# Optimization experiments

Measured on AMD Instinct MI355X. Metric: run time of the kernel, lower is better.

Reference implementation:

```python
import jax, jax.numpy as jnp
import numpy as np

B, C_IN, C_OUT, H, W = 8, 4, 64, 8, 2048


def setup_inputs() -> dict:
    key = jax.random.key(0)
    ks = jax.random.split(key, 7)
    # torch Conv2d default init: U(-s, s) with s = 1/sqrt(fan_in), fan_in = C_in*1*1
    s = 1.0 / np.sqrt(C_IN)
    u = lambda k, shape: jax.random.uniform(k, shape, jnp.float32, -s, s)
    return {
        "x": jax.random.normal(ks[0], (B, C_IN, H, W), jnp.float32),
        "Wq": u(ks[1], (C_OUT, C_IN)), "bq": u(ks[2], (C_OUT,)),
        "Wk": u(ks[3], (C_OUT, C_IN)), "bk": u(ks[4], (C_OUT,)),
        "Wv": u(ks[5], (C_OUT, C_IN)), "bv": u(ks[6], (C_OUT,)),
        "causal": 1,
    }


def reference(x, Wq, bq, Wk, bk, Wv, bv, causal):
    b, c_in, h, w = x.shape
    # 1x1 conv == per-pixel linear over channel axis
    def proj(Wm, bm):
        y = jnp.einsum('bchw,oc->bohw', x, Wm) + bm[None, :, None, None]
        return y.reshape(b, -1, w)              # [B, C_out*H, W]
    Q = proj(Wq, bq)
    K = proj(Wk, bk)
    V = proj(Wv, bv)
    d = Q.shape[1]
    # scores[b,k,l] = sum_d Q[b,d,k] * K[b,d,l] / sqrt(d)   -> [B, W, W]
    scores = jnp.einsum('bdk,bdl->bkl', Q, K) / (float(d) ** 0.5)
    if causal:
        # faithful to torch: triu zeros lower triangle, then any zero -> -inf
        scores = jnp.triu(scores)
        scores = jnp.where(scores != 0, scores, -jnp.inf)
    attn = jax.nn.softmax(scores, axis=-1)
    # x_out[b,d,k] = sum_l V[b,d,l] * attn[b,k,l]
    x_out = jnp.einsum('bdl,bkl->bdk', V, attn).reshape(b, -1, h, w)
    return x_out, scores  # plot_weight is the pre-softmax (masked) scores
```

## Files before the change

kernel.cpp:

```cpp
#include <hip/hip_runtime.h>
#include <math.h>


#define B_ 8
#define W_ 2048
#define D_ 512
#define SCALE_ 0.04419417382415922f
#define NEG_BIG_ (-3.0e38f)

typedef __attribute__((ext_vector_type(8))) short bf16x8;
typedef __attribute__((ext_vector_type(4))) float f32x4;

__device__ __forceinline__ unsigned short f2bf(float x) {
  unsigned int u = __float_as_uint(x);
  u += 0x7fffu + ((u >> 16) & 1u);
  return (unsigned short)(u >> 16);
}
__device__ __forceinline__ float bf2f(unsigned short h) {
  return __uint_as_float(((unsigned int)h) << 16);
}
__device__ __forceinline__ void split2(float x, unsigned short& hi, unsigned short& lo) {
  hi = f2bf(x);
  lo = f2bf(x - bf2f(hi));
}

__device__ __forceinline__ void gl16(const unsigned short* g, unsigned short* l) {
  __builtin_amdgcn_global_load_lds(
      (__attribute__((address_space(1))) void*)const_cast<unsigned short*>(g),
      (__attribute__((address_space(3))) void*)l, 16, 0, 0);
}

__device__ __forceinline__ int swz(int row, int lq) {
  return row * 32 + ((lq ^ ((row >> 1) & 3)) << 3);
}

__global__ __launch_bounds__(256) void proj_qk(
    const float* __restrict__ x,
    const float* __restrict__ Wq, const float* __restrict__ bq,
    const float* __restrict__ Wk, const float* __restrict__ bk,
    unsigned short* __restrict__ Qhi, unsigned short* __restrict__ Qlo,
    unsigned short* __restrict__ Khi, unsigned short* __restrict__ Klo) {
  int idx = blockIdx.x * 256 + threadIdx.x;
  int o = idx & 63;
  int w = (idx >> 6) & (W_ - 1);
  int b = idx >> 17;
  const float* xb = x + (size_t)b * 32 * W_ + w;
  float xv[4][8];
#pragma unroll
  for (int c = 0; c < 4; c++)
#pragma unroll
    for (int h = 0; h < 8; h++) xv[c][h] = xb[(c * 8 + h) * W_];
  float wq0 = Wq[o * 4], wq1 = Wq[o * 4 + 1], wq2 = Wq[o * 4 + 2], wq3 = Wq[o * 4 + 3];
  float wk0 = Wk[o * 4], wk1 = Wk[o * 4 + 1], wk2 = Wk[o * 4 + 2], wk3 = Wk[o * 4 + 3];
  float bqv = bq[o], bkv = bk[o];
  unsigned short qh8[8] __attribute__((aligned(16))), ql8[8] __attribute__((aligned(16)));
  unsigned short kh8[8] __attribute__((aligned(16))), kl8[8] __attribute__((aligned(16)));
#pragma unroll
  for (int h = 0; h < 8; h++) {
    float q = bqv + wq0 * xv[0][h] + wq1 * xv[1][h] + wq2 * xv[2][h] + wq3 * xv[3][h];
    float k = bkv + wk0 * xv[0][h] + wk1 * xv[1][h] + wk2 * xv[2][h] + wk3 * xv[3][h];
    split2(q, qh8[h], ql8[h]);
    split2(k, kh8[h], kl8[h]);
  }
  size_t base = ((size_t)b * W_ + w) * D_ + o * 8;
  *(uint4*)&Qhi[base] = *(uint4*)qh8;
  *(uint4*)&Qlo[base] = *(uint4*)ql8;
  *(uint4*)&Khi[base] = *(uint4*)kh8;
  *(uint4*)&Klo[base] = *(uint4*)kl8;
}

__global__ __launch_bounds__(256) void proj_v(
    const float* __restrict__ x,
    const float* __restrict__ Wv, const float* __restrict__ bv,
    unsigned short* __restrict__ Vhi, unsigned short* __restrict__ Vlo) {
  int idx = blockIdx.x * 256 + threadIdx.x;
  int wc = idx & 255;
  int d = (idx >> 8) & (D_ - 1);
  int b = idx >> 17;
  int o = d >> 3, h = d & 7;
  const float* xp = x + ((size_t)(b * 4) * 8 + h) * W_ + wc * 8;
  float4 xa[4][2];
#pragma unroll
  for (int c = 0; c < 4; c++) {
    xa[c][0] = *(const float4*)&xp[(size_t)c * 8 * W_];
    xa[c][1] = *(const float4*)&xp[(size_t)c * 8 * W_ + 4];
  }
  float w0 = Wv[o * 4], w1 = Wv[o * 4 + 1], w2 = Wv[o * 4 + 2], w3 = Wv[o * 4 + 3];
  float bvv = bv[o];
  unsigned short vh8[8] __attribute__((aligned(16))), vl8[8] __attribute__((aligned(16)));
#pragma unroll
  for (int j = 0; j < 8; j++) {
    float x0 = (j < 4) ? ((const float*)&xa[0][0])[j] : ((const float*)&xa[0][1])[j - 4];
    float x1 = (j < 4) ? ((const float*)&xa[1][0])[j] : ((const float*)&xa[1][1])[j - 4];
    float x2 = (j < 4) ? ((const float*)&xa[2][0])[j] : ((const float*)&xa[2][1])[j - 4];
    float x3 = (j < 4) ? ((const float*)&xa[3][0])[j] : ((const float*)&xa[3][1])[j - 4];
    float v = bvv + w0 * x0 + w1 * x1 + w2 * x2 + w3 * x3;
    split2(v, vh8[j], vl8[j]);
  }
  size_t base = ((size_t)b * D_ + d) * W_ + wc * 8;
  *(uint4*)&Vhi[base] = *(uint4*)vh8;
  *(uint4*)&Vlo[base] = *(uint4*)vl8;
}

__global__ __launch_bounds__(256) void scores_mfma(
    const unsigned short* __restrict__ Qhi, const unsigned short* __restrict__ Qlo,
    const unsigned short* __restrict__ Khi, const unsigned short* __restrict__ Klo,
    float* __restrict__ S, float2* __restrict__ stats, const int* __restrict__ causal_p) {
  int f = (blockIdx.z * 16 + blockIdx.y) * 16 + blockIdx.x;
  int lf = (f & 7) * 256 + (f >> 3);
  int b = lf >> 8;
  int k0 = ((lf >> 4) & 15) * 128;
  int l0 = (lf & 15) * 128;
  int causal = *causal_p;
  int t = threadIdx.x;
  float* Sb = S + (size_t)b * W_ * W_;

  if (causal && (l0 + 127 < k0)) {
    float4 nb = make_float4(NEG_BIG_, NEG_BIG_, NEG_BIG_, NEG_BIG_);
    int row = t >> 1, c0 = (t & 1) * 64;
#pragma unroll
    for (int j = 0; j < 16; j++)
      *(float4*)&Sb[(size_t)(k0 + row) * W_ + l0 + c0 + j * 4] = nb;
    return;
  }

  __shared__ __align__(16) unsigned short qh_s[128 * 32], ql_s[128 * 32];
  __shared__ __align__(16) unsigned short kh_s[128 * 32], kl_s[128 * 32];
  __shared__ float sm_h[2][128], ss_h[2][128];

  int wave = t >> 6, lane = t & 63;
  int wk0 = (wave >> 1) * 64, wl0 = (wave & 1) * 64;
  int lr = lane & 15, lq = lane >> 4;

  const unsigned short* Qhb = Qhi + ((size_t)b * W_ + k0) * D_;
  const unsigned short* Qlb = Qlo + ((size_t)b * W_ + k0) * D_;
  const unsigned short* Khb = Khi + ((size_t)b * W_ + l0) * D_;
  const unsigned short* Klb = Klo + ((size_t)b * W_ + l0) * D_;

  int srow0 = t >> 2, sq = t & 3;
  int srow1 = srow0 + 64;
  size_t g0 = (size_t)srow0 * D_ + ((sq ^ ((srow0 >> 1) & 3)) << 3);
  size_t g1 = (size_t)srow1 * D_ + ((sq ^ ((srow1 >> 1) & 3)) << 3);
  int a0 = t * 8, a1 = t * 8 + 2048;

  f32x4 acc[4][4];
#pragma unroll
  for (int i = 0; i < 4; i++)
#pragma unroll
    for (int j = 0; j < 4; j++) acc[i][j] = (f32x4){0.f, 0.f, 0.f, 0.f};

  for (int d0 = 0; d0 < D_; d0 += 32) {
    gl16(Qhb + g0 + d0, &qh_s[a0]);
    gl16(Qhb + g1 + d0, &qh_s[a1]);
    gl16(Qlb + g0 + d0, &ql_s[a0]);
    gl16(Qlb + g1 + d0, &ql_s[a1]);
    gl16(Khb + g0 + d0, &kh_s[a0]);
    gl16(Khb + g1 + d0, &kh_s[a1]);
    gl16(Klb + g0 + d0, &kl_s[a0]);
    gl16(Klb + g1 + d0, &kl_s[a1]);
    __syncthreads();

    bf16x8 ah[4], al[4], bh[4], bl[4];
#pragma unroll
    for (int mt = 0; mt < 4; mt++) {
      int a = swz(wk0 + mt * 16 + lr, lq);
      ah[mt] = *(const bf16x8*)&qh_s[a];
      al[mt] = *(const bf16x8*)&ql_s[a];
    }
#pragma unroll
    for (int nt = 0; nt < 4; nt++) {
      int a = swz(wl0 + nt * 16 + lr, lq);
      bh[nt] = *(const bf16x8*)&kh_s[a];
      bl[nt] = *(const bf16x8*)&kl_s[a];
    }
    __builtin_amdgcn_s_setprio(1);
#pragma unroll
    for (int mt = 0; mt < 4; mt++)
#pragma unroll
      for (int nt = 0; nt < 4; nt++) {
        acc[mt][nt] = __builtin_amdgcn_mfma_f32_16x16x32_bf16(ah[mt], bh[nt], acc[mt][nt], 0, 0, 0);
        acc[mt][nt] = __builtin_amdgcn_mfma_f32_16x16x32_bf16(ah[mt], bl[nt], acc[mt][nt], 0, 0, 0);
        acc[mt][nt] = __builtin_amdgcn_mfma_f32_16x16x32_bf16(al[mt], bh[nt], acc[mt][nt], 0, 0, 0);
      }
    __builtin_amdgcn_s_setprio(0);
    __syncthreads();
  }

  int wh = wl0 >> 6;
#pragma unroll
  for (int mt = 0; mt < 4; mt++)
#pragma unroll
    for (int r = 0; r < 4; r++) {
      int rr = wk0 + mt * 16 + lq * 4 + r;
      int k = k0 + rr;
      float v4[4];
#pragma unroll
      for (int nt = 0; nt < 4; nt++) {
        int l = l0 + wl0 + nt * 16 + lr;
        float s = acc[mt][nt][r] * SCALE_;
        if (causal && (l < k || s == 0.0f)) s = NEG_BIG_;
        Sb[(size_t)k * W_ + l] = s;
        v4[nt] = s;
      }
      float mx = fmaxf(fmaxf(v4[0], v4[1]), fmaxf(v4[2], v4[3]));
#pragma unroll
      for (int off = 1; off < 16; off <<= 1) mx = fmaxf(mx, __shfl_xor(mx, off, 64));
      float ss = __expf(v4[0] - mx) + __expf(v4[1] - mx) +
                 __expf(v4[2] - mx) + __expf(v4[3] - mx);
#pragma unroll
      for (int off = 1; off < 16; off <<= 1) ss += __shfl_xor(ss, off, 64);
      if (lr == 0) { sm_h[wh][rr] = mx; ss_h[wh][rr] = ss; }
    }
  __syncthreads();
  if (t < 128) {
    float m0 = sm_h[0][t], m1 = sm_h[1][t];
    float s0 = ss_h[0][t], s1 = ss_h[1][t];
    float m = fmaxf(m0, m1);
    float ssum = s0 * __expf(m0 - m) + s1 * __expf(m1 - m);
    stats[((size_t)b * W_ + k0 + t) * 16 + (l0 >> 7)] = make_float2(m, ssum);
  }
}

__global__ __launch_bounds__(256) void combine_stats(
    const float2* __restrict__ stats, float* __restrict__ mrow,
    float* __restrict__ invrow, const int* __restrict__ causal_p) {
  int row = blockIdx.x * 256 + threadIdx.x;
  int k = row & (W_ - 1);
  int lt0 = (*causal_p) ? (k >> 7) : 0;
  const float2* sp = stats + (size_t)row * 16;
  float m = -INFINITY;
  for (int lt = lt0; lt < 16; lt++) m = fmaxf(m, sp[lt].x);
  float s = 0.f;
  for (int lt = lt0; lt < 16; lt++) s += sp[lt].y * __expf(sp[lt].x - m);
  mrow[row] = m;
  invrow[row] = 1.0f / s;
}

__global__ __launch_bounds__(256) void out_bal(
    const unsigned short* __restrict__ Vhi, const unsigned short* __restrict__ Vlo,
    const float* __restrict__ S,
    const float* __restrict__ mrow, const float* __restrict__ invrow,
    float* __restrict__ O, const int* __restrict__ causal_p) {
  int f = blockIdx.z * 64 + blockIdx.x;
  int lf = (f & 7) * 64 + (f >> 3);
  int b = lf >> 6;
  int j2 = lf & 63;
  int k0 = (j2 >> 2) * 128;
  int dq = j2 & 3;
  int causal = *causal_p;
  int t = threadIdx.x;
  int wave = t >> 6, lane = t & 63;
  int wd0 = (wave >> 1) * 64;
  int wk0 = (wave & 1) * 64;
  int lr = lane & 15, lq = lane >> 4;

  __shared__ __align__(16) unsigned short vh_s[2][128 * 32], vl_s[2][128 * 32];
  __shared__ __align__(16) unsigned short ph_s[2][128 * 32], pl_s[2][128 * 32];

  const unsigned short* Vhb = Vhi + ((size_t)b * D_ + dq * 128) * W_;
  const unsigned short* Vlb = Vlo + ((size_t)b * D_ + dq * 128) * W_;
  const float* Sb = S + (size_t)b * W_ * W_;

  int rA = t >> 2, qc = t & 3;
  int vx = (qc ^ ((rA >> 1) & 3)) << 3;
  const unsigned short* VhA = Vhb + (size_t)rA * W_ + vx;
  const unsigned short* VhB = VhA + (size_t)64 * W_;
  const unsigned short* VlA = Vlb + (size_t)rA * W_ + vx;
  const unsigned short* VlB = VlA + (size_t)64 * W_;
  int a0 = t * 8, a1 = t * 8 + 2048;

  const float* SrowA = Sb + (size_t)(k0 + rA) * W_ + qc * 8;
  const float* SrowB = SrowA + (size_t)64 * W_;
  int pA = rA * 32 + vx;
  int pB = pA + 64 * 32;
  float mA = mrow[(size_t)b * W_ + k0 + rA], iA = invrow[(size_t)b * W_ + k0 + rA];
  float mB = mrow[(size_t)b * W_ + k0 + rA + 64], iB = invrow[(size_t)b * W_ + k0 + rA + 64];

  f32x4 acc[4][4];
#pragma unroll
  for (int i = 0; i < 4; i++)
#pragma unroll
    for (int j = 0; j < 4; j++) acc[i][j] = (f32x4){0.f, 0.f, 0.f, 0.f};

  int lstart = causal ? k0 : 0;
  int nch = (W_ - lstart) >> 5;

  auto stageV = [&](int buf, int l) {
    gl16(VhA + l, &vh_s[buf][a0]);
    gl16(VhB + l, &vh_s[buf][a1]);
    gl16(VlA + l, &vl_s[buf][a0]);
    gl16(VlB + l, &vl_s[buf][a1]);
  };
  auto writeP = [&](unsigned short* __restrict__ ph, unsigned short* __restrict__ pl,
                    float4 sa0, float4 sa1, float4 sb0, float4 sb1) {
    float p[8];
    unsigned short hi8[8] __attribute__((aligned(16)));
    unsigned short lo8[8] __attribute__((aligned(16)));
    p[0] = __expf(sa0.x - mA) * iA; p[1] = __expf(sa0.y - mA) * iA;
    p[2] = __expf(sa0.z - mA) * iA; p[3] = __expf(sa0.w - mA) * iA;
    p[4] = __expf(sa1.x - mA) * iA; p[5] = __expf(sa1.y - mA) * iA;
    p[6] = __expf(sa1.z - mA) * iA; p[7] = __expf(sa1.w - mA) * iA;
#pragma unroll
    for (int j = 0; j < 8; j++) split2(p[j], hi8[j], lo8[j]);
    *(uint4*)&ph[pA] = *(uint4*)hi8;
    *(uint4*)&pl[pA] = *(uint4*)lo8;
    p[0] = __expf(sb0.x - mB) * iB; p[1] = __expf(sb0.y - mB) * iB;
    p[2] = __expf(sb0.z - mB) * iB; p[3] = __expf(sb0.w - mB) * iB;
    p[4] = __expf(sb1.x - mB) * iB; p[5] = __expf(sb1.y - mB) * iB;
    p[6] = __expf(sb1.z - mB) * iB; p[7] = __expf(sb1.w - mB) * iB;
#pragma unroll
    for (int j = 0; j < 8; j++) split2(p[j], hi8[j], lo8[j]);
    *(uint4*)&ph[pB] = *(uint4*)hi8;
    *(uint4*)&pl[pB] = *(uint4*)lo8;
  };
  auto compute = [&](const unsigned short* vh, const unsigned short* vl,
                     const unsigned short* ph, const unsigned short* pl) {
    bf16x8 ah[4], al[4], bh[4], bl[4];
#pragma unroll
    for (int mt = 0; mt < 4; mt++) {
      int a = swz(wd0 + mt * 16 + lr, lq);
      ah[mt] = *(const bf16x8*)&vh[a];
      al[mt] = *(const bf16x8*)&vl[a];
    }
#pragma unroll
    for (int nt = 0; nt < 4; nt++) {
      int a = swz(wk0 + nt * 16 + lr, lq);
      bh[nt] = *(const bf16x8*)&ph[a];
      bl[nt] = *(const bf16x8*)&pl[a];
    }
    __builtin_amdgcn_s_setprio(1);
#pragma unroll
    for (int mt = 0; mt < 4; mt++)
#pragma unroll
      for (int nt = 0; nt < 4; nt++) {
        acc[mt][nt] = __builtin_amdgcn_mfma_f32_16x16x32_bf16(ah[mt], bh[nt], acc[mt][nt], 0, 0, 0);
        acc[mt][nt] = __builtin_amdgcn_mfma_f32_16x16x32_bf16(ah[mt], bl[nt], acc[mt][nt], 0, 0, 0);
        acc[mt][nt] = __builtin_amdgcn_mfma_f32_16x16x32_bf16(al[mt], bh[nt], acc[mt][nt], 0, 0, 0);
      }
    __builtin_amdgcn_s_setprio(0);
  };

  float4 sAE0, sAE1, sBE0, sBE1, sAO0, sAO1, sBO0, sBO1;

  sAE0 = *(const float4*)&SrowA[lstart];      sAE1 = *(const float4*)&SrowA[lstart + 4];
  sBE0 = *(const float4*)&SrowB[lstart];      sBE1 = *(const float4*)&SrowB[lstart + 4];
  sAO0 = *(const float4*)&SrowA[lstart + 32]; sAO1 = *(const float4*)&SrowA[lstart + 36];
  sBO0 = *(const float4*)&SrowB[lstart + 32]; sBO1 = *(const float4*)&SrowB[lstart + 36];
  stageV(0, lstart);
  writeP(&ph_s[0][0], &pl_s[0][0], sAE0, sAE1, sBE0, sBE1);
  __syncthreads();

  for (int ci = 0; ci < nch; ci += 2) {
    int base = lstart + ci * 32;
    if (ci + 2 < nch) {
      sAE0 = *(const float4*)&SrowA[base + 64]; sAE1 = *(const float4*)&SrowA[base + 68];
      sBE0 = *(const float4*)&SrowB[base + 64]; sBE1 = *(const float4*)&SrowB[base + 68];
    }
    stageV(1, base + 32);
    writeP(&ph_s[1][0], &pl_s[1][0], sAO0, sAO1, sBO0, sBO1);
    compute(&vh_s[0][0], &vl_s[0][0], &ph_s[0][0], &pl_s[0][0]);
    __syncthreads();
    bool more = (ci + 2 < nch);
    if (ci + 3 < nch) {
      sAO0 = *(const float4*)&SrowA[base + 96]; sAO1 = *(const float4*)&SrowA[base + 100];
      sBO0 = *(const float4*)&SrowB[base + 96]; sBO1 = *(const float4*)&SrowB[base + 100];
    }
    if (more) {
      stageV(0, base + 64);
      writeP(&ph_s[0][0], &pl_s[0][0], sAE0, sAE1, sBE0, sBE1);
    }
    compute(&vh_s[1][0], &vl_s[1][0], &ph_s[1][0], &pl_s[1][0]);
    __syncthreads();
  }

#pragma unroll
  for (int mt = 0; mt < 4; mt++)
#pragma unroll
    for (int nt = 0; nt < 4; nt++)
#pragma unroll
      for (int r = 0; r < 4; r++) {
        int d = dq * 128 + wd0 + mt * 16 + lq * 4 + r;
        int k = k0 + wk0 + nt * 16 + lr;
        O[((size_t)b * D_ + d) * W_ + k] = acc[mt][nt][r];
      }
}

extern "C" void kernel_launch(void* const* d_in, const int* in_sizes, int n_in,
                              void* d_out, int out_size, void* d_ws, size_t ws_size,
                              hipStream_t stream) {
  const float* x  = (const float*)d_in[0];
  const float* Wq = (const float*)d_in[1];
  const float* bq = (const float*)d_in[2];
  const float* Wk = (const float*)d_in[3];
  const float* bk = (const float*)d_in[4];
  const float* Wv = (const float*)d_in[5];
  const float* bv = (const float*)d_in[6];
  const int* causal = (const int*)d_in[7];

  float* out = (float*)d_out;
  float* x_out = out;
  float* S = out + (size_t)B_ * D_ * W_;

  const size_t NQ = (size_t)B_ * W_ * D_;
  unsigned short* wsu = (unsigned short*)d_ws;
  unsigned short* Qhi = wsu;
  unsigned short* Qlo = wsu + NQ;
  unsigned short* Khi = wsu + 2 * NQ;
  unsigned short* Klo = wsu + 3 * NQ;
  unsigned short* Vhi = wsu + 4 * NQ;
  unsigned short* Vlo = wsu + 5 * NQ;
  float* mrow   = (float*)(wsu + 6 * NQ);
  float* invrow = mrow + (size_t)B_ * W_;
  float2* stats = (float2*)(invrow + (size_t)B_ * W_);

  proj_qk<<<4096, 256, 0, stream>>>(x, Wq, bq, Wk, bk, Qhi, Qlo, Khi, Klo);
  proj_v<<<4096, 256, 0, stream>>>(x, Wv, bv, Vhi, Vlo);
  scores_mfma<<<dim3(16, 16, B_), 256, 0, stream>>>(Qhi, Qlo, Khi, Klo, S, stats, causal);
  combine_stats<<<64, 256, 0, stream>>>(stats, mrow, invrow, causal);
  out_bal<<<dim3(64, 1, B_), 256, 0, stream>>>(Vhi, Vlo, S, mrow, invrow, x_out, causal);
}
```

Baseline: 370.1 us.

## Double-buffer scores LDS staging, merge projection kernels, fold stats combine into output

The scores kernel now double-buffers its Q/K hi/lo LDS tiles, issuing async loads for the next d-chunk before running MFMAs on the current one, so global loads can overlap compute. The two projection kernels become one launch, split by block index. The combine_stats kernel is removed, and each out_bal block reduces the per-tile softmax stats for its own rows. This saves two launches but doubles LDS use in the scores kernel, which may lower occupancy, and duplicates the stats reduction across the d-quarter blocks.

Result: no change. 371.7 us (+0.4%).

```diff
diff --git a/kernel.cpp b/kernel.cpp
--- a/kernel.cpp
+++ b/kernel.cpp
@@ -34,72 +34,72 @@
   return row * 32 + ((lq ^ ((row >> 1) & 3)) << 3);
 }
 
-__global__ __launch_bounds__(256) void proj_qk(
+__global__ __launch_bounds__(256) void proj_all(
     const float* __restrict__ x,
     const float* __restrict__ Wq, const float* __restrict__ bq,
     const float* __restrict__ Wk, const float* __restrict__ bk,
+    const float* __restrict__ Wv, const float* __restrict__ bv,
     unsigned short* __restrict__ Qhi, unsigned short* __restrict__ Qlo,
-    unsigned short* __restrict__ Khi, unsigned short* __restrict__ Klo) {
-  int idx = blockIdx.x * 256 + threadIdx.x;
-  int o = idx & 63;
-  int w = (idx >> 6) & (W_ - 1);
-  int b = idx >> 17;
-  const float* xb = x + (size_t)b * 32 * W_ + w;
-  float xv[4][8];
-#pragma unroll
-  for (int c = 0; c < 4; c++)
-#pragma unroll
-    for (int h = 0; h < 8; h++) xv[c][h] = xb[(c * 8 + h) * W_];
-  float wq0 = Wq[o * 4], wq1 = Wq[o * 4 + 1], wq2 = Wq[o * 4 + 2], wq3 = Wq[o * 4 + 3];
-  float wk0 = Wk[o * 4], wk1 = Wk[o * 4 + 1], wk2 = Wk[o * 4 + 2], wk3 = Wk[o * 4 + 3];
-  float bqv = bq[o], bkv = bk[o];
-  unsigned short qh8[8] __attribute__((aligned(16))), ql8[8] __attribute__((aligned(16)));
-  unsigned short kh8[8] __attribute__((aligned(16))), kl8[8] __attribute__((aligned(16)));
-#pragma unroll
-  for (int h = 0; h < 8; h++) {
-    float q = bqv + wq0 * xv[0][h] + wq1 * xv[1][h] + wq2 * xv[2][h] + wq3 * xv[3][h];
-    float k = bkv + wk0 * xv[0][h] + wk1 * xv[1][h] + wk2 * xv[2][h] + wk3 * xv[3][h];
-    split2(q, qh8[h], ql8[h]);
-    split2(k, kh8[h], kl8[h]);
+    unsigned short* __restrict__ Khi, unsigned short* __restrict__ Klo,
+    unsigned short* __restrict__ Vhi, unsigned short* __restrict__ Vlo) {
+  int bid = blockIdx.x;
+  if (bid < 4096) {
+    int idx = bid * 256 + threadIdx.x;
+    int o = idx & 63;
+    int w = (idx >> 6) & (W_ - 1);
+    int b = idx >> 17;
+    const float* xb = x + (size_t)b * 32 * W_ + w;
+    float xv[4][8];
+#pragma unroll
+    for (int c = 0; c < 4; c++)
+#pragma unroll
+      for (int h = 0; h < 8; h++) xv[c][h] = xb[(c * 8 + h) * W_];
+    float wq0 = Wq[o * 4], wq1 = Wq[o * 4 + 1], wq2 = Wq[o * 4 + 2], wq3 = Wq[o * 4 + 3];
+    float wk0 = Wk[o * 4], wk1 = Wk[o * 4 + 1], wk2 = Wk[o * 4 + 2], wk3 = Wk[o * 4 + 3];
+    float bqv = bq[o], bkv = bk[o];
+    unsigned short qh8[8] __attribute__((aligned(16))), ql8[8] __attribute__((aligned(16)));
+    unsigned short kh8[8] __attribute__((aligned(16))), kl8[8] __attribute__((aligned(16)));
+#pragma unroll
+    for (int h = 0; h < 8; h++) {
+      float q = bqv + wq0 * xv[0][h] + wq1 * xv[1][h] + wq2 * xv[2][h] + wq3 * xv[3][h];
+      float k = bkv + wk0 * xv[0][h] + wk1 * xv[1][h] + wk2 * xv[2][h] + wk3 * xv[3][h];
+      split2(q, qh8[h], ql8[h]);
+      split2(k, kh8[h], kl8[h]);
+    }
+    size_t base = ((size_t)b * W_ + w) * D_ + o * 8;
+    *(uint4*)&Qhi[base] = *(uint4*)qh8;
+    *(uint4*)&Qlo[base] = *(uint4*)ql8;
+    *(uint4*)&Khi[base] = *(uint4*)kh8;
+    *(uint4*)&Klo[base] = *(uint4*)kl8;
+  } else {
+    int idx = (bid - 4096) * 256 + threadIdx.x;
+    int wc = idx & 255;
+    int d = (idx >> 8) & (D_ - 1);
+    int b = idx >> 17;
+    int o = d >> 3, h = d & 7;
+    const float* xp = x + ((size_t)(b * 4) * 8 + h) * W_ + wc * 8;
+    float4 xa[4][2];
+#pragma unroll
+    for (int c = 0; c < 4; c++) {
+      xa[c][0] = *(const float4*)&xp[(size_t)c * 8 * W_];
+      xa[c][1] = *(const float4*)&xp[(size_t)c * 8 * W_ + 4];
+    }
+    float w0 = Wv[o * 4], w1 = Wv[o * 4 + 1], w2 = Wv[o * 4 + 2], w3 = Wv[o * 4 + 3];
+    float bvv = bv[o];
+    unsigned short vh8[8] __attribute__((aligned(16))), vl8[8] __attribute__((aligned(16)));
+#pragma unroll
+    for (int j = 0; j < 8; j++) {
+      float x0 = (j < 4) ? ((const float*)&xa[0][0])[j] : ((const float*)&xa[0][1])[j - 4];
+      float x1 = (j < 4) ? ((const float*)&xa[1][0])[j] : ((const float*)&xa[1][1])[j - 4];
+      float x2 = (j < 4) ? ((const float*)&xa[2][0])[j] : ((const float*)&xa[2][1])[j - 4];
+      float x3 = (j < 4) ? ((const float*)&xa[3][0])[j] : ((const float*)&xa[3][1])[j - 4];
+      float v = bvv + w0 * x0 + w1 * x1 + w2 * x2 + w3 * x3;
+      split2(v, vh8[j], vl8[j]);
+    }
+    size_t base = ((size_t)b * D_ + d) * W_ + wc * 8;
+    *(uint4*)&Vhi[base] = *(uint4*)vh8;
+    *(uint4*)&Vlo[base] = *(uint4*)vl8;
   }
-  size_t base = ((size_t)b * W_ + w) * D_ + o * 8;
-  *(uint4*)&Qhi[base] = *(uint4*)qh8;
-  *(uint4*)&Qlo[base] = *(uint4*)ql8;
-  *(uint4*)&Khi[base] = *(uint4*)kh8;
-  *(uint4*)&Klo[base] = *(uint4*)kl8;
-}
-
-__global__ __launch_bounds__(256) void proj_v(
-    const float* __restrict__ x,
-    const float* __restrict__ Wv, const float* __restrict__ bv,
-    unsigned short* __restrict__ Vhi, unsigned short* __restrict__ Vlo) {
-  int idx = blockIdx.x * 256 + threadIdx.x;
-  int wc = idx & 255;
-  int d = (idx >> 8) & (D_ - 1);
-  int b = idx >> 17;
-  int o = d >> 3, h = d & 7;
-  const float* xp = x + ((size_t)(b * 4) * 8 + h) * W_ + wc * 8;
-  float4 xa[4][2];
-#pragma unroll
-  for (int c = 0; c < 4; c++) {
-    xa[c][0] = *(const float4*)&xp[(size_t)c * 8 * W_];
-    xa[c][1] = *(const float4*)&xp[(size_t)c * 8 * W_ + 4];
-  }
-  float w0 = Wv[o * 4], w1 = Wv[o * 4 + 1], w2 = Wv[o * 4 + 2], w3 = Wv[o * 4 + 3];
-  float bvv = bv[o];
-  unsigned short vh8[8] __attribute__((aligned(16))), vl8[8] __attribute__((aligned(16)));
-#pragma unroll
-  for (int j = 0; j < 8; j++) {
-    float x0 = (j < 4) ? ((const float*)&xa[0][0])[j] : ((const float*)&xa[0][1])[j - 4];
-    float x1 = (j < 4) ? ((const float*)&xa[1][0])[j] : ((const float*)&xa[1][1])[j - 4];
-    float x2 = (j < 4) ? ((const float*)&xa[2][0])[j] : ((const float*)&xa[2][1])[j - 4];
-    float x3 = (j < 4) ? ((const float*)&xa[3][0])[j] : ((const float*)&xa[3][1])[j - 4];
-    float v = bvv + w0 * x0 + w1 * x1 + w2 * x2 + w3 * x3;
-    split2(v, vh8[j], vl8[j]);
-  }
-  size_t base = ((size_t)b * D_ + d) * W_ + wc * 8;
-  *(uint4*)&Vhi[base] = *(uint4*)vh8;
-  *(uint4*)&Vlo[base] = *(uint4*)vl8;
 }
 
 __global__ __launch_bounds__(256) void scores_mfma(
@@ -124,8 +124,8 @@
     return;
   }
 
-  __shared__ __align__(16) unsigned short qh_s[128 * 32], ql_s[128 * 32];
-  __shared__ __align__(16) unsigned short kh_s[128 * 32], kl_s[128 * 32];
+  __shared__ __align__(16) unsigned short qh_s[2][4096], ql_s[2][4096];
+  __shared__ __align__(16) unsigned short kh_s[2][4096], kl_s[2][4096];
   __shared__ float sm_h[2][128], ss_h[2][128];
 
   int wave = t >> 6, lane = t & 63;
@@ -143,35 +143,42 @@
   size_t g1 = (size_t)srow1 * D_ + ((sq ^ ((srow1 >> 1) & 3)) << 3);
   int a0 = t * 8, a1 = t * 8 + 2048;
 
+  auto stage = [&](int buf, int d0) {
+    gl16(Qhb + g0 + d0, &qh_s[buf][a0]);
+    gl16(Qhb + g1 + d0, &qh_s[buf][a1]);
+    gl16(Qlb + g0 + d0, &ql_s[buf][a0]);
+    gl16(Qlb + g1 + d0, &ql_s[buf][a1]);
+    gl16(Khb + g0 + d0, &kh_s[buf][a0]);
+    gl16(Khb + g1 + d0, &kh_s[buf][a1]);
+    gl16(Klb + g0 + d0, &kl_s[buf][a0]);
+    gl16(Klb + g1 + d0, &kl_s[buf][a1]);
+  };
+
   f32x4 acc[4][4];
 #pragma unroll
   for (int i = 0; i < 4; i++)
 #pragma unroll
     for (int j = 0; j < 4; j++) acc[i][j] = (f32x4){0.f, 0.f, 0.f, 0.f};
 
-  for (int d0 = 0; d0 < D_; d0 += 32) {
-    gl16(Qhb + g0 + d0, &qh_s[a0]);
-    gl16(Qhb + g1 + d0, &qh_s[a1]);
-    gl16(Qlb + g0 + d0, &ql_s[a0]);
-    gl16(Qlb + g1 + d0, &ql_s[a1]);
-    gl16(Khb + g0 + d0, &kh_s[a0]);
-    gl16(Khb + g1 + d0, &kh_s[a1]);
-    gl16(Klb + g0 + d0, &kl_s[a0]);
-    gl16(Klb + g1 + d0, &kl_s[a1]);
-    __syncthreads();
+  stage(0, 0);
+  __syncthreads();
+
+  for (int i = 0; i < 16; i++) {
+    int cur = i & 1;
+    if (i < 15) stage(cur ^ 1, (i + 1) * 32);
 
     bf16x8 ah[4], al[4], bh[4], bl[4];
 #pragma unroll
     for (int mt = 0; mt < 4; mt++) {
       int a = swz(wk0 + mt * 16 + lr, lq);
-      ah[mt] = *(const bf16x8*)&qh_s[a];
-      al[mt] = *(const bf16x8*)&ql_s[a];
+      ah[mt] = *(const bf16x8*)&qh_s[cur][a];
+      al[mt] = *(const bf16x8*)&ql_s[cur][a];
     }
 #pragma unroll
     for (int nt = 0; nt < 4; nt++) {
       int a = swz(wl0 + nt * 16 + lr, lq);
-      bh[nt] = *(const bf16x8*)&kh_s[a];
-      bl[nt] = *(const bf16x8*)&kl_s[a];
+      bh[nt] = *(const bf16x8*)&kh_s[cur][a];
+      bl[nt] = *(const bf16x8*)&kl_s[cur][a];
     }
     __builtin_amdgcn_s_setprio(1);
 #pragma unroll
@@ -221,25 +228,9 @@
   }
 }
 
-__global__ __launch_bounds__(256) void combine_stats(
-    const float2* __restrict__ stats, float* __restrict__ mrow,
-    float* __restrict__ invrow, const int* __restrict__ causal_p) {
-  int row = blockIdx.x * 256 + threadIdx.x;
-  int k = row & (W_ - 1);
-  int lt0 = (*causal_p) ? (k >> 7) : 0;
-  const float2* sp = stats + (size_t)row * 16;
-  float m = -INFINITY;
-  for (int lt = lt0; lt < 16; lt++) m = fmaxf(m, sp[lt].x);
-  float s = 0.f;
-  for (int lt = lt0; lt < 16; lt++) s += sp[lt].y * __expf(sp[lt].x - m);
-  mrow[row] = m;
-  invrow[row] = 1.0f / s;
-}
-
 __global__ __launch_bounds__(256) void out_bal(
     const unsigned short* __restrict__ Vhi, const unsigned short* __restrict__ Vlo,
-    const float* __restrict__ S,
-    const float* __restrict__ mrow, const float* __restrict__ invrow,
+    const float* __restrict__ S, const float2* __restrict__ stats,
     float* __restrict__ O, const int* __restrict__ causal_p) {
   int f = blockIdx.z * 64 + blockIdx.x;
   int lf = (f & 7) * 64 + (f >> 3);
@@ -273,8 +264,17 @@
   const float* SrowB = SrowA + (size_t)64 * W_;
   int pA = rA * 32 + vx;
   int pB = pA + 64 * 32;
-  float mA = mrow[(size_t)b * W_ + k0 + rA], iA = invrow[(size_t)b * W_ + k0 + rA];
-  float mB = mrow[(size_t)b * W_ + k0 + rA + 64], iB = invrow[(size_t)b * W_ + k0 + rA + 64];
+
+  int lt0 = causal ? (k0 >> 7) : 0;
+  const float2* spA = stats + ((size_t)b * W_ + k0 + rA) * 16;
+  const float2* spB = spA + 64 * 16;
+  float mA = -INFINITY, mB = -INFINITY;
+  for (int lt = lt0; lt < 16; lt++) mA = fmaxf(mA, spA[lt].x);
+  for (int lt = lt0; lt < 16; lt++) mB = fmaxf(mB, spB[lt].x);
+  float sA = 0.f, sB = 0.f;
+  for (int lt = lt0; lt < 16; lt++) sA += spA[lt].y * __expf(spA[lt].x - mA);
+  for (int lt = lt0; lt < 16; lt++) sB += spB[lt].y * __expf(spB[lt].x - mB);
+  float iA = 1.0f / sA, iB = 1.0f / sB;
 
   f32x4 acc[4][4];
 #pragma unroll
@@ -409,13 +409,10 @@
   unsigned short* Klo = wsu + 3 * NQ;
   unsigned short* Vhi = wsu + 4 * NQ;
   unsigned short* Vlo = wsu + 5 * NQ;
-  float* mrow   = (float*)(wsu + 6 * NQ);
-  float* invrow = mrow + (size_t)B_ * W_;
-  float2* stats = (float2*)(invrow + (size_t)B_ * W_);
-
-  proj_qk<<<4096, 256, 0, stream>>>(x, Wq, bq, Wk, bk, Qhi, Qlo, Khi, Klo);
-  proj_v<<<4096, 256, 0, stream>>>(x, Wv, bv, Vhi, Vlo);
+  float2* stats = (float2*)(wsu + 6 * NQ);
+
+  proj_all<<<8192, 256, 0, stream>>>(x, Wq, bq, Wk, bk, Wv, bv,
+                                     Qhi, Qlo, Khi, Klo, Vhi, Vlo);
   scores_mfma<<<dim3(16, 16, B_), 256, 0, stream>>>(Qhi, Qlo, Khi, Klo, S, stats, causal);
-  combine_stats<<<64, 256, 0, stream>>>(stats, mrow, invrow, causal);
-  out_bal<<<dim3(64, 1, B_), 256, 0, stream>>>(Vhi, Vlo, S, mrow, invrow, x_out, causal);
-}
+  out_bal<<<dim3(64, 1, B_), 256, 0, stream>>>(Vhi, Vlo, S, stats, x_out, causal);
+}
```
